# Kernel optimization log

Measured on AMD Instinct MI355X. Metric: run time of the kernel, lower is better.

## Reference

```python
import jax, jax.numpy as jnp
import numpy as np

VOXEL_SIZE = jnp.array([0.075, 0.075], dtype=jnp.float32)
PC_RANGE = jnp.array([-54.0, -54.0], dtype=jnp.float32)
FUSION_STRIDE = 8.0
SRC_STRIDES = (4.0, 8.0)
RADII = (2.4, 4.8)
NSAMPLE = 16
NKEY = 500


def _mlp(x, w1, g1, b1, w2, b2):
    # Linear(no bias) + BatchNorm(eval, running mean=0/var=1 -> affine) + ReLU, then Linear
    h = jax.nn.relu((x @ w1) * g1 + b1)
    return h @ w2 + b2


def _world(coords, stride):
    # voxel coord -> world xy center
    return (coords.astype(jnp.float32) + 0.5) * stride * VOXEL_SIZE + PC_RANGE


def _gather_rows(x, idx):
    # x: (B, N, ...), idx: (B, ...) -> per-batch row gather
    return jax.vmap(lambda f, i: f[i])(x, idx)


def _knn(key_world, src_world, src_feat, radius):
    # key_world (B,Nk,2), src_world (B,Ns,2), src_feat (B,Ns,C)
    d2 = jnp.sum((key_world[:, :, None, :] - src_world[:, None, :, :]) ** 2, axis=-1)  # (B,Nk,Ns)
    d2 = jnp.where(d2 <= radius * radius, d2, jnp.inf)
    negd, idx = jax.lax.top_k(-d2, NSAMPLE)  # nearest NSAMPLE within radius, (B,Nk,K)
    valid = jnp.isfinite(negd).astype(src_feat.dtype)  # empty==0 mask
    feats = _gather_rows(src_feat, idx)  # (B,Nk,K,C)
    return feats * valid[..., None]


def setup_inputs() -> dict:
    key = jax.random.key(0)
    ks = jax.random.split(key, 24)
    s = 0.05
    return {
        'fusion_feat': jax.random.normal(ks[0], (2, 20000, 128), jnp.float32),
        'src_feat_a': jax.random.normal(ks[1], (2, 30000, 128), jnp.float32),
        'src_feat_b': jax.random.normal(ks[2], (2, 30000, 128), jnp.float32),
        'heat_w1': jax.random.normal(ks[3], (128, 128), jnp.float32) * s,
        'heat_g1': jnp.ones((128,), jnp.float32),
        'heat_b1': jnp.zeros((128,), jnp.float32),
        'heat_w2': jax.random.normal(ks[4], (128, 10), jnp.float32) * s,
        'heat_b2': jnp.zeros((10,), jnp.float32),
        'knn_w': jax.random.normal(ks[5], (2, 16), jnp.float32) * s,
        'knn_b': jnp.zeros((2,), jnp.float32),
        'kw_w1': jax.random.normal(ks[6], (128, 64), jnp.float32) * s,
        'kw_g1': jnp.ones((64,), jnp.float32),
        'kw_b1': jnp.zeros((64,), jnp.float32),
        'kw_w2': jax.random.normal(ks[7], (64, 3), jnp.float32) * s,
        'kw_b2': jnp.zeros((3,), jnp.float32),
        'fuse_w1': jax.random.normal(ks[8], (256, 256), jnp.float32) * s,
        'fuse_g1': jnp.ones((256,), jnp.float32),
        'fuse_b1': jnp.zeros((256,), jnp.float32),
        'fuse_w2': jax.random.normal(ks[9], (256, 128), jnp.float32) * s,
        'fuse_b2': jnp.zeros((128,), jnp.float32),
        'fusion_coords': jax.random.randint(ks[10], (2, 20000, 2), 0, 180, jnp.int32),
        'src_coords_a': jax.random.randint(ks[11], (2, 30000, 2), 0, 360, jnp.int32),
        'src_coords_b': jax.random.randint(ks[12], (2, 30000, 2), 0, 180, jnp.int32),
    }


def reference(fusion_feat, src_feat_a, src_feat_b, heat_w1, heat_g1, heat_b1,
              heat_w2, heat_b2, knn_w, knn_b, kw_w1, kw_g1, kw_b1, kw_w2, kw_b2,
              fuse_w1, fuse_g1, fuse_b1, fuse_w2, fuse_b2,
              fusion_coords, src_coords_a, src_coords_b):
    B = fusion_feat.shape[0]
    # heatmap head over all fusion voxels
    scores10 = _mlp(fusion_feat, heat_w1, heat_g1, heat_b1, heat_w2, heat_b2)  # (B,Nf,10)
    heat_scores = jnp.max(scores10, axis=-1)
    cls = jnp.argmax(scores10, axis=-1)
    # per-sample top-k key voxel selection
    _, tki = jax.lax.top_k(jax.nn.sigmoid(heat_scores), NKEY)  # (B,Nk)
    key_feat = _gather_rows(fusion_feat, tki)      # (B,Nk,128)
    key_coords = _gather_rows(fusion_coords, tki)  # (B,Nk,2)
    key_class = _gather_rows(cls, tki)             # (B,Nk)
    key_world = _world(key_coords, FUSION_STRIDE)  # (B,Nk,2)

    srcs = ((src_feat_a, src_coords_a), (src_feat_b, src_coords_b))
    mlp_feats = []
    for s, (sf, sc) in enumerate(srcs):
        sw = _world(sc, SRC_STRIDES[s])
        kf = _knn(key_world, sw, sf, RADII[s])  # (B,Nk,K,C), zeroed where empty
        # Linear over the K neighbor axis (knn_feat_mlp: NSAMPLE -> 1)
        mf = jnp.einsum('bnkc,k->bnc', kf, knn_w[s]) + knn_b[s]
        mlp_feats.append(mf)

    w = jax.nn.softmax(_mlp(key_feat, kw_w1, kw_g1, kw_b1, kw_w2, kw_b2), axis=-1)  # (B,Nk,3)
    # faithful to original: key_voxel_feat is re-scaled cumulatively inside the loop
    kvf = key_feat
    fuse_sum = jnp.zeros_like(key_feat)
    for i in range(len(srcs)):
        kvf = w[..., i:i + 1] * kvf
        fuse_sum = fuse_sum + kvf * mlp_feats[i]
    fused = jnp.concatenate([fuse_sum, kvf], axis=-1)  # (B,Nk,256)
    out = _mlp(fused, fuse_w1, fuse_g1, fuse_b1, fuse_w2, fuse_b2)  # (B,Nk,128)

    bs_col = jnp.broadcast_to(jnp.arange(B, dtype=key_coords.dtype)[:, None, None], (B, NKEY, 1))
    key_voxel_indices = jnp.concatenate([bs_col, key_coords], axis=-1).reshape(B * NKEY, 3)
    return (out.reshape(B * NKEY, -1), key_voxel_indices,
            heat_scores.reshape(-1), scores10.reshape(-1, scores10.shape[-1]), key_class)
```

## Files before the change

### kernel.cpp

```cpp
#include <hip/hip_runtime.h>
#include <math.h>

#define BB 2
#define NF 20000
#define NS 30000
#define CH 128
#define NK 500
#define KNN 16
#define KPB 4

#define HA 2.4024f
#define HB 4.8048f
#define NCA 45
#define NCB 23
#define CELLS_A 2025
#define CELLS_B 529

#define GB 8
#define SLICE 3750
#define SLICE4 1875

#define OUT0_OFF 0
#define OUT1_OFF 128000
#define OUT2_OFF 131000
#define OUT3_OFF 171000
#define OUT4_OFF 571000

#define WS_CLS   0
#define WS_TKI   160000
#define WS_KW    164000
#define WS_MF    172000
#define WS_KEYS  WS_MF
#define WS_BH    492000
#define WS_RAWK  754144
#define WS_GSTART 1196000
#define WS_PTS    1236880
#define WS_PIDX   2196880

#define STB(s,b)  ((s) ? (4052 + (b) * 530) : ((b) * 2026))

__device__ __forceinline__ void fma4(float4& acc, float sc, const float4& wv) {
    acc.x += sc * wv.x; acc.y += sc * wv.y;
    acc.z += sc * wv.z; acc.w += sc * wv.w;
}

__device__ __forceinline__ unsigned ordf(float s) {
    unsigned u = __float_as_uint(s);
    return (u & 0x80000000u) ? ~u : (u | 0x80000000u);
}

__device__ __forceinline__ int cell_of(int cxi, int cyi, float stride, float inv_h,
                                       int nc, float& sx, float& sy)
{
    sx = __fadd_rn(__fmul_rn(__fmul_rn(__fadd_rn((float)cxi, 0.5f), stride), 0.075f), -54.0f);
    sy = __fadd_rn(__fmul_rn(__fmul_rn(__fadd_rn((float)cyi, 0.5f), stride), 0.075f), -54.0f);
    int cx = (int)floorf((sx + 54.0f) * inv_h);
    int cy = (int)floorf((sy + 54.0f) * inv_h);
    cx = min(max(cx, 0), nc - 1);
    cy = min(max(cy, 0), nc - 1);
    return cy * nc + cx;
}

__device__ __forceinline__ unsigned block_scan_incl(unsigned v, int tid,
                                                    volatile unsigned* ws,
                                                    unsigned* total)
{
    const int lane = tid & 63, wid = tid >> 6;
    unsigned p = v;
#pragma unroll
    for (int off = 1; off < 64; off <<= 1) {
        unsigned t = (unsigned)__shfl_up((int)p, off);
        if (lane >= off) p += t;
    }
    __syncthreads();
    if (lane == 63) ws[wid] = p;
    __syncthreads();
    unsigned woff = 0, tot = 0;
#pragma unroll
    for (int w = 0; w < 16; ++w) {
        unsigned s = ws[w];
        tot += s;
        if (w < wid) woff += s;
    }
    *total = tot;
    return p + woff;
}

__global__ __launch_bounds__(256) void heat_kernel(
    const float* __restrict__ x,
    const float* __restrict__ w1,
// ... 115 lines not shown
    }
    __syncthreads();

    const int r = tid >> 2;
    const int p = tid & 3;
    float a2[10];
#pragma unroll
    for (int c = 0; c < 10; ++c) a2[c] = 0.f;
    for (int kk = 0; kk < 32; ++kk) {
        int k = kk * 4 + p;
        float hv = Hs[r * 132 + k];
#pragma unroll
        for (int c = 0; c < 10; ++c) a2[c] += hv * W2s[k * 10 + c];
    }
#pragma unroll
    for (int c = 0; c < 10; ++c) {
        a2[c] += __shfl_xor(a2[c], 1);
        a2[c] += __shfl_xor(a2[c], 2);
    }
    if (p == 0) {
        int m = m0 + r;
        float best = -INFINITY;
        int bi = 0;
#pragma unroll
        for (int c = 0; c < 10; ++c) {
            float s = a2[c] + b2[c];
            out_s10[(size_t)m * 10 + c] = s;
            if (s > best) { best = s; bi = c; }
        }
        out_heat[m] = best;
        cls[m] = bi;
        int b = m / NF;
        unsigned i = (unsigned)(m - b * NF);
        float sig = 1.0f / (1.0f + expf(-best));
        keys[m] = ((unsigned long long)ordf(sig) << 32) | (unsigned)(~i);
        rawk[m] = ordf(best);
    }
}

#define H1BINS 16384

__global__ __launch_bounds__(1024) void mid_kernel(
    const unsigned long long* __restrict__ keys,
    const unsigned* __restrict__ rawk,
    const int* __restrict__ cls,
    const int* __restrict__ fcoords,
    float* __restrict__ out1,
    float* __restrict__ out4,
    int* __restrict__ tki,
    float* __restrict__ keyworld,
    const int* __restrict__ sca, const int* __restrict__ scb,
    const int* __restrict__ bh,
    int* __restrict__ gstart,
    float2* __restrict__ pts, int* __restrict__ pidx)
{
    __shared__ unsigned h[H1BINS];
    __shared__ unsigned long long list[1024];
    __shared__ unsigned short bins16[NF];
    __shared__ unsigned wsum[16];
    __shared__ unsigned chunk_s, aboveC_s, T1_s, aboveT1_s, cand_s, thr_s, cnt_s;
    const int tid = threadIdx.x;
    const int blk = blockIdx.x;

    if (blk >= 2) {
        const int idx = blk - 2;
        const int sb = idx >> 3;
        const int j = idx & (GB - 1);
        const int s = sb >> 1, b = sb & 1;
        const int n = s ? CELLS_B : CELLS_A;
        const int nc = s ? NCB : NCA;
        const float stride = s ? 8.0f : 4.0f;
        const float inv_h = s ? (1.0f / HB) : (1.0f / HA);
        const int stb = STB(s, b);
        const int2* sc = ((const int2*)(s ? scb : sca)) + (size_t)b * NS;
        const int4* scv = (const int4*)sc;
        const size_t pbase = ((size_t)s * BB + b) * NS;
        const int* bhsb = bh + (sb << 14);
        int* tot = (int*)h;
        int* cur = ((int*)h) + 2048;

        for (int c = tid; c < 2048; c += 1024) {
            int t = 0, pr = 0;
#pragma unroll
            for (int g = 0; g < GB; ++g) {
                int v = bhsb[(g << 11) + c];
                t += v;
                if (g < j) pr += v;
            }
            tot[c] = t;
            cur[c] = pr;
        }
        __syncthreads();
        const int i0 = tid * 2, i1 = tid * 2 + 1;
        int c0 = (i0 < n) ? tot[i0] : 0;
        int c1 = (i1 < n) ? tot[i1] : 0;
        unsigned totsum;
        unsigned P = block_scan_incl((unsigned)(c0 + c1), tid, wsum, &totsum);
        const int excl = (int)P - (c0 + c1);
        if (i0 < n) {
            if (j == 0) gstart[stb + i0] = excl;
            cur[i0] += excl;
        }
        if (i1 < n) {
            if (j == 0) gstart[stb + i1] = excl + c0;
            cur[i1] += excl + c0;
        }
        if (j == 0 && tid == 0) gstart[stb + n] = NS;
        __syncthreads();
        for (int p = j * SLICE4 + tid; p < (j + 1) * SLICE4; p += 1024) {
            int4 v = scv[p];
            float sx0, sy0, sx1, sy1;
            int cell0 = cell_of(v.x, v.y, stride, inv_h, nc, sx0, sy0);
            int cell1 = cell_of(v.z, v.w, stride, inv_h, nc, sx1, sy1);
            int pos0 = atomicAdd(&cur[cell0], 1);
            int pos1 = atomicAdd(&cur[cell1], 1);
            pts[pbase + pos0] = make_float2(sx0, sy0);
            pidx[pbase + pos0] = p * 2;
            pts[pbase + pos1] = make_float2(sx1, sy1);
            pidx[pbase + pos1] = p * 2 + 1;
        }
        return;
    }

    const int b = blk;
    const unsigned long long* kb = keys + (size_t)b * NF;
    const unsigned* rk = rawk + (size_t)b * NF;
    const unsigned K = NK;

    for (int i = tid; i < H1BINS; i += 1024) h[i] = 0u;
    __syncthreads();
    for (int i2 = tid; i2 < NF / 2; i2 += 1024) {
        uint2 rv = ((const uint2*)rk)[i2];
        unsigned b0 = rv.x >> 18;
        unsigned b1_ = rv.y >> 18;
        bins16[2 * i2] = (unsigned short)b0;
        bins16[2 * i2 + 1] = (unsigned short)b1_;
        atomicAdd(&h[b0], 1u);
        atomicAdd(&h[b1_], 1u);
    }
    __syncthreads();
    unsigned ck = 0;
    {
        int base = tid * 16;
#pragma unroll
        for (int j = 0; j < 16; ++j) ck += h[base + j];
    }
    {
        unsigned tot;
        unsigned P = block_scan_incl(ck, tid, wsum, &tot);
        unsigned suf = tot - P + ck;
        unsigned above = tot - P;
        if (above < K && K <= suf) { chunk_s = (unsigned)tid; aboveC_s = above; }
    }
    __syncthreads();
    if (tid == 0) {
        int bin = (int)chunk_s * 16 + 15;
        unsigned acc = aboveC_s;
        for (;; --bin) { if (acc + h[bin] >= K) break; acc += h[bin]; }
        T1_s = (unsigned)bin;
        aboveT1_s = acc;
        cand_s = acc + h[bin];
        cnt_s = 0u;
    }
    __syncthreads();
    const unsigned T1 = T1_s;

    if (cand_s <= 1024u) {
        const unsigned* b32v = (const unsigned*)bins16;
        for (int i2 = tid; i2 < NF / 2; i2 += 1024) {
            unsigned pk = b32v[i2];
            if ((pk & 0xFFFFu) >= T1) {
                unsigned pos = atomicAdd(&cnt_s, 1u);
                if (pos < 1024u) list[pos] = kb[2 * i2];
            }
            if ((pk >> 16) >= T1) {
                unsigned pos = atomicAdd(&cnt_s, 1u);
                if (pos < 1024u) list[pos] = kb[2 * i2 + 1];
            }
        }
    } else {
// ... 2 lines not shown
        __syncthreads();
#pragma unroll 4
        for (int i = tid; i < NF; i += 1024) {
            unsigned rw = rk[i];
            if ((rw >> 18) == T1)
                atomicAdd(&h[(rw >> 8) & 1023u], 1u);
        }
        __syncthreads();
        unsigned hb = h[tid];
        {
            unsigned tot2;
            unsigned P2 = block_scan_incl(hb, tid, wsum, &tot2);
            unsigned suf = tot2 - P2 + hb;
            unsigned above = tot2 - P2;
            if (above < K2 && K2 <= suf) thr_s = (T1 << 10) | (unsigned)tid;
        }
        __syncthreads();
        const unsigned thr24 = thr_s;
#pragma unroll 4
        for (int i = tid; i < NF; i += 1024) {
            unsigned rw = rk[i];
            if ((rw >> 8) >= thr24) {
                unsigned pos = atomicAdd(&cnt_s, 1u);
                if (pos < 1024u) list[pos] = kb[i];
            }
        }
    }
    __syncthreads();
    const int cc = (int)(cnt_s > 1024u ? 1024u : cnt_s);

    if (tid < cc) {
        unsigned long long mykey = list[tid];
        unsigned r = 0;
#pragma unroll 8
        for (int j = 0; j < cc; ++j) r += (list[j] > mykey) ? 1u : 0u;
        if (r < (unsigned)NK) {
            int idx = (int)(~(unsigned)(mykey & 0xFFFFFFFFull));
            tki[b * NK + (int)r] = idx;
            int c0 = fcoords[((size_t)b * NF + idx) * 2 + 0];
            int c1 = fcoords[((size_t)b * NF + idx) * 2 + 1];
            size_t o = (size_t)(b * NK + (int)r);
            out1[o * 3 + 0] = (float)b;
            out1[o * 3 + 1] = (float)c0;
            out1[o * 3 + 2] = (float)c1;
            float wx = __fadd_rn(__fmul_rn(__fmul_rn(__fadd_rn((float)c0, 0.5f), 8.0f), 0.075f), -54.0f);
            float wy = __fadd_rn(__fmul_rn(__fmul_rn(__fadd_rn((float)c1, 0.5f), 8.0f), 0.075f), -54.0f);
            keyworld[o * 2 + 0] = wx;
            keyworld[o * 2 + 1] = wy;
            out4[o] = (float)cls[(size_t)b * NF + idx];
        }
    }
}

__global__ __launch_bounds__(256) void knn_kernel(
    const float* __restrict__ sfa, const float* __restrict__ sfb,
    const int* __restrict__ gstart,
    const float2* __restrict__ pts, const int* __restrict__ pidx,
    const float* __restrict__ knn_w,
    const float* __restrict__ knn_b,
    const float* __restrict__ keyworld,
    float* __restrict__ mf)
{
    __shared__ unsigned long long list[1024];
    __shared__ float psum[128];
    __shared__ unsigned cnt_s;
    const int tid = threadIdx.x;
    const int blk = blockIdx.x;
    const int s = blk / (BB * NK);
    const int rest = blk % (BB * NK);
    const int b = rest / NK;
    const int r = rest % NK;
    const float* sfeat = s ? sfb : sfa;
    const float r2 = s ? (float)(4.8 * 4.8) : (float)(2.4 * 2.4);
    const float inv_h = s ? (1.0f / HB) : (1.0f / HA);
    const int nc = s ? NCB : NCA;
    const int stb = STB(s, b);
    const size_t pbase = ((size_t)s * BB + b) * NS;

    if (tid == 0) cnt_s = 0u;
    __syncthreads();
    const float kx = keyworld[((size_t)b * NK + r) * 2 + 0];
    const float ky = keyworld[((size_t)b * NK + r) * 2 + 1];
    int cx = (int)floorf((kx + 54.0f) * inv_h);
    int cy = (int)floorf((ky + 54.0f) * inv_h);
    cx = min(max(cx, 0), nc - 1);
    cy = min(max(cy, 0), nc - 1);
    const int c0 = max(cx - 1, 0), c1 = min(cx + 1, nc - 1);
    const int cy0 = max(cy - 1, 0), cy1 = min(cy + 1, nc - 1);

    for (int cyy = cy0; cyy <= cy1; ++cyy) {
        int lo = gstart[stb + cyy * nc + c0];
        int hi = gstart[stb + cyy * nc + c1 + 1];
        for (int p = lo + tid; p < hi; p += 256) {
            float2 w = pts[pbase + p];
            float dx = __fsub_rn(kx, w.x);
            float dy = __fsub_rn(ky, w.y);
            float d2 = __fadd_rn(__fmul_rn(dx, dx), __fmul_rn(dy, dy));
            if (d2 <= r2) {
                unsigned pos = atomicAdd(&cnt_s, 1u);
                if (pos < 1024u)
                    list[pos] = ((unsigned long long)__float_as_uint(d2) << 32)
                              | (unsigned)pidx[pbase + p];
            }
        }
    }
    __syncthreads();
    int cc = (int)cnt_s;
    if (cc > 1024) cc = 1024;
    int n2 = 16;
    while (n2 < cc) n2 <<= 1;
    for (int i = tid; i < n2; i += 256)
        if (i >= cc) list[i] = ~0ull;
    __syncthreads();
    for (int kk = 2; kk <= n2; kk <<= 1) {
        for (int j = kk >> 1; j > 0; j >>= 1) {
            for (int i = tid; i < n2; i += 256) {
                int ixj = i ^ j;
                if (ixj > i) {
                    unsigned long long a = list[i], bv = list[ixj];
                    bool up = ((i & kk) == 0);
                    bool sw = up ? (a > bv) : (a < bv);
                    if (sw) { list[i] = bv; list[ixj] = a; }
                }
            }
            __syncthreads();
        }
    }
    {
        int K = cc < KNN ? cc : KNN;
        int col = tid & 127, half = tid >> 7;
        float acc = 0.f;
        int k0 = half * 8, k1 = min(K, half * 8 + 8);
        for (int k = k0; k < k1; ++k) {
            unsigned i = (unsigned)(list[k] & 0xFFFFFFFFull);
            acc += knn_w[s * 16 + k] * sfeat[((size_t)b * NS + i) * CH + col];
        }
        if (half) psum[col] = acc;
        __syncthreads();
        if (!half)
            mf[(((size_t)s * BB + b) * NK + r) * CH + col] = knn_b[s] + acc + psum[col];
    }
}

__global__ __launch_bounds__(1024) void fuse_kernel(
    const float* __restrict__ ffeat,
    const int* __restrict__ tki,
    const float* __restrict__ kw_w1, const float* __restrict__ kw_g1,
    const float* __restrict__ kw_b1, const float* __restrict__ kw_w2,
    const float* __restrict__ kw_b2,
    const float* __restrict__ fuse_w1, const float* __restrict__ fuse_g1,
    const float* __restrict__ fuse_b1, const float* __restrict__ fuse_w2,
    const float* __restrict__ fuse_b2,
    const float* __restrict__ mf,
    float* __restrict__ out0)
{
    __shared__ float pL[16384];
    __shared__ float xsT[512];
    __shared__ float mfs[1024];
    __shared__ float fusedvT[1024];
    __shared__ float h2sT[1024];
    __shared__ float prm[964];
    __shared__ float hsX[256];
    __shared__ float p2[96];
    __shared__ float l3[12];
    __shared__ float wsm[8];
    __shared__ int idxs[KPB], bs[KPB], rs[KPB];
    const int tid = threadIdx.x;
    const int f0 = blockIdx.x * KPB;

    if (tid < 964) {
        float v;
        if (tid < 64)       v = kw_g1[tid];
        else if (tid < 128) v = kw_b1[tid - 64];
        else if (tid < 320) v = kw_w2[tid - 128];
        else if (tid < 323) v = kw_b2[tid - 320];
        else if (tid < 324) v = 0.f;
        else if (tid < 580) v = fuse_g1[tid - 324];
        else if (tid < 836) v = fuse_b1[tid - 580];
        else                v = fuse_b2[tid - 836];
        prm[tid] = v;
    }
    if (tid < KPB) {
        int flat = f0 + tid;
        int b = flat / NK;
        bs[tid] = b;
        rs[tid] = flat - b * NK;
        idxs[tid] = tki[flat];
    }
    __syncthreads();

    if (tid < 128) {
        int key = tid >> 5, c4 = tid & 31;
        float4 v = ((const float4*)(ffeat + ((size_t)bs[key] * NF + idxs[key]) * CH))[c4];
        xsT[(c4 * 4 + 0) * 4 + key] = v.x;
        xsT[(c4 * 4 + 1) * 4 + key] = v.y;
        xsT[(c4 * 4 + 2) * 4 + key] = v.z;
        xsT[(c4 * 4 + 3) * 4 + key] = v.w;
    }
    if (tid < 256) {
        int ss = tid >> 7, key = (tid >> 5) & 3, c4 = tid & 31;
        float4 v = ((const float4*)(mf + (((size_t)ss * BB + bs[key]) * NK + rs[key]) * CH))[c4];
        *(float4*)&mfs[ss * 512 + key * 128 + c4 * 4] = v;
    }
    __syncthreads();

    if (tid < 256) {
        const int og = tid & 15, kseg = tid >> 4;
        float4 wr[8];
#pragma unroll
        for (int m = 0; m < 8; ++m)
            wr[m] = ((const float4*)kw_w1)[(kseg * 8 + m) * 16 + og];
        float4 a0 = {0, 0, 0, 0}, a1 = {0, 0, 0, 0}, a2 = {0, 0, 0, 0}, a3 = {0, 0, 0, 0};
#pragma unroll
        for (int m = 0; m < 8; ++m) {
            float4 f4 = *(const float4*)&xsT[(kseg * 8 + m) * 4];
            fma4(a0, f4.x, wr[m]);
            fma4(a1, f4.y, wr[m]);
            fma4(a2, f4.z, wr[m]);
            fma4(a3, f4.w, wr[m]);
        }
        *(float4*)&pL[(kseg * 4 + 0) * 64 + og * 4] = a0;
        *(float4*)&pL[(kseg * 4 + 1) * 64 + og * 4] = a1;
        *(float4*)&pL[(kseg * 4 + 2) * 64 + og * 4] = a2;
        *(float4*)&pL[(kseg * 4 + 3) * 64 + og * 4] = a3;
    }
    __syncthreads();
    if (tid < 256) {
        int out = tid >> 2, key = tid & 3;
        float s = 0.f;
#pragma unroll
        for (int ks = 0; ks < 16; ++ks) s += pL[(ks * 4 + key) * 64 + out];
        float t = s * prm[out] + prm[64 + out];
        hsX[key * 64 + out] = t > 0.f ? t : 0.f;
    }
    __syncthreads();
    if (tid < 96) {
        int key = tid / 24, rr = tid % 24, out = rr >> 3, seg = rr & 7;
        float acc = 0.f;
#pragma unroll
        for (int m = 0; m < 8; ++m) {
            int k = seg * 8 + m;
            acc += hsX[key * 64 + k] * prm[128 + k * 3 + out];
        }
        p2[(key * 3 + out) * 8 + seg] = acc;
    }
    __syncthreads();
    if (tid < 12) {
        int key = tid / 3, out = tid % 3;
        float s = 0.f;
#pragma unroll
        for (int j = 0; j < 8; ++j) s += p2[(key * 3 + out) * 8 + j];
        l3[key * 3 + out] = s + prm[320 + out];
    }
    __syncthreads();
    if (tid < KPB) {
        float l0 = l3[tid * 3], l1 = l3[tid * 3 + 1], l2 = l3[tid * 3 + 2];
        float m = fmaxf(l0, fmaxf(l1, l2));
        float e0 = expf(l0 - m), e1 = expf(l1 - m), e2 = expf(l2 - m);
        float sum = e0 + e1 + e2;
        wsm[tid * 2 + 0] = e0 / sum;
        wsm[tid * 2 + 1] = e1 / sum;
    }
    __syncthreads();

    {
        int c = tid >> 2, key = tid & 3;
        float w0 = wsm[key * 2], w1_ = wsm[key * 2 + 1];
        float val;
        if (c < 128) {
            float xv_ = xsT[c * 4 + key];
            float m0 = mfs[key * 128 + c];
            float m1 = mfs[512 + key * 128 + c];
            float kv = w0 * xv_;
            float kv2 = w1_ * kv;
            val = kv * m0 + kv2 * m1;
        } else {
            float xv_ = xsT[(c - 128) * 4 + key];
            val = w1_ * (w0 * xv_);
        }
        fusedvT[tid] = val;
    }
    __syncthreads();

    {
        const int og = tid & 63, kseg = tid >> 6;
        const float4* w1v = (const float4*)fuse_w1;
        float4 wr[16];
#pragma unroll
        for (int m = 0; m < 16; ++m)
            wr[m] = w1v[(kseg * 16 + m) * 64 + og];
        float4 a0 = {0, 0, 0, 0}, a1 = {0, 0, 0, 0}, a2 = {0, 0, 0, 0}, a3 = {0, 0, 0, 0};
#pragma unroll
        for (int m = 0; m < 16; ++m) {
            float4 f4 = *(const float4*)&fusedvT[(kseg * 16 + m) * 4];
            fma4(a0, f4.x, wr[m]);
            fma4(a1, f4.y, wr[m]);
            fma4(a2, f4.z, wr[m]);
            fma4(a3, f4.w, wr[m]);
        }
        *(float4*)&pL[(kseg * 4 + 0) * 256 + og * 4] = a0;
        *(float4*)&pL[(kseg * 4 + 1) * 256 + og * 4] = a1;
        *(float4*)&pL[(kseg * 4 + 2) * 256 + og * 4] = a2;
        *(float4*)&pL[(kseg * 4 + 3) * 256 + og * 4] = a3;
    }
    __syncthreads();
    {
        int out = tid >> 2, key = tid & 3;
        float s = 0.f;
#pragma unroll
        for (int ks = 0; ks < 16; ++ks) s += pL[(ks * 4 + key) * 256 + out];
        float t = s * prm[324 + out] + prm[580 + out];
        h2sT[out * 4 + key] = t > 0.f ? t : 0.f;
    }
    __syncthreads();

    {
        const int og2 = tid & 31, kseg2 = tid >> 5;
        const float4* w2v = (const float4*)fuse_w2;
        float4 wr[8];
#pragma unroll
        for (int m = 0; m < 8; ++m)
            wr[m] = w2v[(kseg2 * 8 + m) * 32 + og2];
        float4 a0 = {0, 0, 0, 0}, a1 = {0, 0, 0, 0}, a2 = {0, 0, 0, 0}, a3 = {0, 0, 0, 0};
#pragma unroll
        for (int m = 0; m < 8; ++m) {
            float4 f4 = *(const float4*)&h2sT[(kseg2 * 8 + m) * 4];
            fma4(a0, f4.x, wr[m]);
            fma4(a1, f4.y, wr[m]);
            fma4(a2, f4.z, wr[m]);
            fma4(a3, f4.w, wr[m]);
        }
        *(float4*)&pL[(kseg2 * 4 + 0) * 128 + og2 * 4] = a0;
        *(float4*)&pL[(kseg2 * 4 + 1) * 128 + og2 * 4] = a1;
        *(float4*)&pL[(kseg2 * 4 + 2) * 128 + og2 * 4] = a2;
        *(float4*)&pL[(kseg2 * 4 + 3) * 128 + og2 * 4] = a3;
    }
    __syncthreads();
    if (tid < 512) {
        int out = tid >> 2, key = tid & 3;
        float s = prm[836 + out];
#pragma unroll
        for (int ks = 0; ks < 32; ++ks) s += pL[(ks * 4 + key) * 128 + out];
        out0[((size_t)bs[key] * NK + rs[key]) * CH + out] = s;
    }
}

extern "C" void kernel_launch(void* const* d_in, const int* in_sizes, int n_in,
                              void* d_out, int out_size, void* d_ws, size_t ws_size,
                              hipStream_t stream)
{
    const float* fusion_feat = (const float*)d_in[0];
    const float* src_feat_a  = (const float*)d_in[1];
    const float* src_feat_b  = (const float*)d_in[2];
    const float* heat_w1 = (const float*)d_in[3];
    const float* heat_g1 = (const float*)d_in[4];
    const float* heat_b1 = (const float*)d_in[5];
    const float* heat_w2 = (const float*)d_in[6];
    const float* heat_b2 = (const float*)d_in[7];
    const float* knn_w   = (const float*)d_in[8];
    const float* knn_b   = (const float*)d_in[9];
    const float* kw_w1   = (const float*)d_in[10];
    const float* kw_g1   = (const float*)d_in[11];
    const float* kw_b1   = (const float*)d_in[12];
    const float* kw_w2   = (const float*)d_in[13];
    const float* kw_b2   = (const float*)d_in[14];
    const float* fuse_w1 = (const float*)d_in[15];
    const float* fuse_g1 = (const float*)d_in[16];
    const float* fuse_b1 = (const float*)d_in[17];
    const float* fuse_w2 = (const float*)d_in[18];
    const float* fuse_b2 = (const float*)d_in[19];
    const int* fusion_coords = (const int*)d_in[20];
    const int* src_coords_a  = (const int*)d_in[21];
    const int* src_coords_b  = (const int*)d_in[22];

    float* out = (float*)d_out;
    char* ws = (char*)d_ws;
    int* cls = (int*)(ws + WS_CLS);
    int* tki = (int*)(ws + WS_TKI);
    float* keyworld = (float*)(ws + WS_KW);
    float* mf = (float*)(ws + WS_MF);
    unsigned long long* keys = (unsigned long long*)(ws + WS_KEYS);
    int* bh = (int*)(ws + WS_BH);
    unsigned* rawk = (unsigned*)(ws + WS_RAWK);
    int* gstart = (int*)(ws + WS_GSTART);
    float2* pts = (float2*)(ws + WS_PTS);
    int* pidx = (int*)(ws + WS_PIDX);

    heat_kernel<<<(BB * NF) / 64 + 4 * GB, 256, 0, stream>>>(
        fusion_feat, heat_w1, heat_g1, heat_b1, heat_w2, heat_b2,
        out + OUT2_OFF, out + OUT3_OFF, cls, keys,
        src_coords_a, src_coords_b, bh, rawk);

    mid_kernel<<<2 + 4 * GB, 1024, 0, stream>>>(
        keys, rawk, cls, fusion_coords,
        out + OUT1_OFF, out + OUT4_OFF, tki, keyworld,
        src_coords_a, src_coords_b, bh, gstart, pts, pidx);

    knn_kernel<<<2 * BB * NK, 256, 0, stream>>>(
        src_feat_a, src_feat_b, gstart, pts, pidx,
        knn_w, knn_b, keyworld, mf);

    fuse_kernel<<<(BB * NK) / KPB, 1024, 0, stream>>>(
        fusion_feat, tki, kw_w1, kw_g1, kw_b1, kw_w2, kw_b2,
        fuse_w1, fuse_g1, fuse_b1, fuse_w2, fuse_b2, mf, out + OUT0_OFF);
}
```

Measured before the change: 218.5 us.

## Fuse fuse MLP into knn kernel via per-key completion counter

Removes the separate fuse_kernel launch. Each knn block atomically increments a per-key counter, which mid_kernel resets. The second block to finish for a key (covering both source scales) runs the key-weight MLP, softmax, fusion and two-layer MLP for that single key using 256 threads. This saves a kernel launch and the tail gap between launches. In exchange, weights are no longer shared across four keys per block, so fuse_w1 and fuse_w2 are reloaded per key, and a serial tail of matrix work now runs inside the last-finishing knn blocks.

Result: slower. 438.6 us (+100.7%).

```diff
diff --git a/kernel.cpp b/kernel.cpp
--- a/kernel.cpp
+++ b/kernel.cpp
@@ -7,7 +7,6 @@
 #define CH 128
 #define NK 500
 #define KNN 16
-#define KPB 4
 
 #define HA 2.4024f
 #define HB 4.8048f
@@ -36,6 +35,7 @@
 #define WS_GSTART 1196000
 #define WS_PTS    1236880
 #define WS_PIDX   2196880
+#define WS_KDONE  2676880
 
 #define STB(s,b)  ((s) ? (4052 + (b) * 530) : ((b) * 2026))
 
@@ -257,7 +257,8 @@
     const int* __restrict__ sca, const int* __restrict__ scb,
     const int* __restrict__ bh,
     int* __restrict__ gstart,
-    float2* __restrict__ pts, int* __restrict__ pidx)
+    float2* __restrict__ pts, int* __restrict__ pidx,
+    unsigned* __restrict__ kdone)
 {
     __shared__ unsigned h[H1BINS];
     __shared__ unsigned long long list[1024];
@@ -331,6 +332,8 @@
     const unsigned long long* kb = keys + (size_t)b * NF;
     const unsigned* rk = rawk + (size_t)b * NF;
     const unsigned K = NK;
+
+    if (tid < NK) kdone[b * NK + tid] = 0u;
 
     for (int i = tid; i < H1BINS; i += 1024) h[i] = 0u;
     __syncthreads();
@@ -446,11 +449,34 @@
     const float* __restrict__ knn_w,
     const float* __restrict__ knn_b,
     const float* __restrict__ keyworld,
-    float* __restrict__ mf)
+    float* __restrict__ mf,
+    const float* __restrict__ ffeat,
+    const int* __restrict__ tki,
+    const float* __restrict__ kw_w1, const float* __restrict__ kw_g1,
+    const float* __restrict__ kw_b1, const float* __restrict__ kw_w2,
+    const float* __restrict__ kw_b2,
+    const float* __restrict__ fuse_w1, const float* __restrict__ fuse_g1,
+    const float* __restrict__ fuse_b1, const float* __restrict__ fuse_w2,
+    const float* __restrict__ fuse_b2,
+    unsigned* __restrict__ kdone,
+    float* __restrict__ out0)
 {
-    __shared__ unsigned long long list[1024];
+    __shared__ union {
+        unsigned long long list[1024];
+        struct {
+            float prm[964];
+            float xs[128];
+            float mfs[256];
+            float fusedv[256];
+            float hs[64];
+            float h2[256];
+        } f;
+    } u;
+    __shared__ float pbuf[1024];
     __shared__ float psum[128];
+    __shared__ float p2[24], l3[3], wsm[2];
     __shared__ unsigned cnt_s;
+    __shared__ int old_s;
     const int tid = threadIdx.x;
     const int blk = blockIdx.x;
     const int s = blk / (BB * NK);
@@ -486,8 +512,8 @@
             if (d2 <= r2) {
                 unsigned pos = atomicAdd(&cnt_s, 1u);
                 if (pos < 1024u)
-                    list[pos] = ((unsigned long long)__float_as_uint(d2) << 32)
-                              | (unsigned)pidx[pbase + p];
+                    u.list[pos] = ((unsigned long long)__float_as_uint(d2) << 32)
+                                | (unsigned)pidx[pbase + p];
             }
         }
     }
@@ -497,17 +523,17 @@
     int n2 = 16;
     while (n2 < cc) n2 <<= 1;
     for (int i = tid; i < n2; i += 256)
-        if (i >= cc) list[i] = ~0ull;
+        if (i >= cc) u.list[i] = ~0ull;
     __syncthreads();
     for (int kk = 2; kk <= n2; kk <<= 1) {
         for (int j = kk >> 1; j > 0; j >>= 1) {
             for (int i = tid; i < n2; i += 256) {
                 int ixj = i ^ j;
                 if (ixj > i) {
-                    unsigned long long a = list[i], bv = list[ixj];
+                    unsigned long long a = u.list[i], bv = u.list[ixj];
                     bool up = ((i & kk) == 0);
                     bool sw = up ? (a > bv) : (a < bv);
-                    if (sw) { list[i] = bv; list[ixj] = a; }
+                    if (sw) { u.list[i] = bv; u.list[ixj] = a; }
                 }
             }
             __syncthreads();
@@ -519,7 +545,7 @@
         float acc = 0.f;
         int k0 = half * 8, k1 = min(K, half * 8 + 8);
         for (int k = k0; k < k1; ++k) {
-            unsigned i = (unsigned)(list[k] & 0xFFFFFFFFull);
+            unsigned i = (unsigned)(u.list[k] & 0xFFFFFFFFull);
             acc += knn_w[s * 16 + k] * sfeat[((size_t)b * NS + i) * CH + col];
         }
         if (half) psum[col] = acc;
@@ -527,208 +553,133 @@
         if (!half)
             mf[(((size_t)s * BB + b) * NK + r) * CH + col] = knn_b[s] + acc + psum[col];
     }
-}
-
-__global__ __launch_bounds__(1024) void fuse_kernel(
-    const float* __restrict__ ffeat,
-    const int* __restrict__ tki,
-    const float* __restrict__ kw_w1, const float* __restrict__ kw_g1,
-    const float* __restrict__ kw_b1, const float* __restrict__ kw_w2,
-    const float* __restrict__ kw_b2,
-    const float* __restrict__ fuse_w1, const float* __restrict__ fuse_g1,
-    const float* __restrict__ fuse_b1, const float* __restrict__ fuse_w2,
-    const float* __restrict__ fuse_b2,
-    const float* __restrict__ mf,
-    float* __restrict__ out0)
-{
-    __shared__ float pL[16384];
-    __shared__ float xsT[512];
-    __shared__ float mfs[1024];
-    __shared__ float fusedvT[1024];
-    __shared__ float h2sT[1024];
-    __shared__ float prm[964];
-    __shared__ float hsX[256];
-    __shared__ float p2[96];
-    __shared__ float l3[12];
-    __shared__ float wsm[8];
-    __shared__ int idxs[KPB], bs[KPB], rs[KPB];
-    const int tid = threadIdx.x;
-    const int f0 = blockIdx.x * KPB;
-
-    if (tid < 964) {
+
+    __syncthreads();
+    __threadfence();
+    if (tid == 0) old_s = (int)atomicAdd(&kdone[b * NK + r], 1u);
+    __syncthreads();
+    if (old_s != 1) return;
+    __threadfence();
+
+    for (int i = tid; i < 964; i += 256) {
         float v;
-        if (tid < 64)       v = kw_g1[tid];
-        else if (tid < 128) v = kw_b1[tid - 64];
-        else if (tid < 320) v = kw_w2[tid - 128];
-        else if (tid < 323) v = kw_b2[tid - 320];
-        else if (tid < 324) v = 0.f;
-        else if (tid < 580) v = fuse_g1[tid - 324];
-        else if (tid < 836) v = fuse_b1[tid - 580];
-        else                v = fuse_b2[tid - 836];
-        prm[tid] = v;
-    }
-    if (tid < KPB) {
-        int flat = f0 + tid;
-        int b = flat / NK;
-        bs[tid] = b;
-        rs[tid] = flat - b * NK;
-        idxs[tid] = tki[flat];
-    }
-    __syncthreads();
-
-    if (tid < 128) {
-        int key = tid >> 5, c4 = tid & 31;
-        float4 v = ((const float4*)(ffeat + ((size_t)bs[key] * NF + idxs[key]) * CH))[c4];
-        xsT[(c4 * 4 + 0) * 4 + key] = v.x;
-        xsT[(c4 * 4 + 1) * 4 + key] = v.y;
-        xsT[(c4 * 4 + 2) * 4 + key] = v.z;
-        xsT[(c4 * 4 + 3) * 4 + key] = v.w;
-    }
-    if (tid < 256) {
-        int ss = tid >> 7, key = (tid >> 5) & 3, c4 = tid & 31;
-        float4 v = ((const float4*)(mf + (((size_t)ss * BB + bs[key]) * NK + rs[key]) * CH))[c4];
-        *(float4*)&mfs[ss * 512 + key * 128 + c4 * 4] = v;
-    }
-    __syncthreads();
-
-    if (tid < 256) {
+        if (i < 64)       v = kw_g1[i];
+        else if (i < 128) v = kw_b1[i - 64];
+        else if (i < 320) v = kw_w2[i - 128];
+        else if (i < 323) v = kw_b2[i - 320];
+        else if (i < 324) v = 0.f;
+        else if (i < 580) v = fuse_g1[i - 324];
+        else if (i < 836) v = fuse_b1[i - 580];
+        else              v = fuse_b2[i - 836];
+        u.f.prm[i] = v;
+    }
+    const int kidx = tki[b * NK + r];
+    if (tid < 32) {
+        float4 v = ((const float4*)(ffeat + ((size_t)b * NF + kidx) * CH))[tid];
+        *(float4*)&u.f.xs[tid * 4] = v;
+    }
+    if (tid < 64) {
+        int ss = tid >> 5, c4 = tid & 31;
+        float4 v = ((const float4*)(mf + (((size_t)ss * BB + b) * NK + r) * CH))[c4];
+        *(float4*)&u.f.mfs[ss * 128 + c4 * 4] = v;
+    }
+    __syncthreads();
+
+    {
         const int og = tid & 15, kseg = tid >> 4;
-        float4 wr[8];
-#pragma unroll
-        for (int m = 0; m < 8; ++m)
-            wr[m] = ((const float4*)kw_w1)[(kseg * 8 + m) * 16 + og];
-        float4 a0 = {0, 0, 0, 0}, a1 = {0, 0, 0, 0}, a2 = {0, 0, 0, 0}, a3 = {0, 0, 0, 0};
+        float4 a = {0, 0, 0, 0};
 #pragma unroll
         for (int m = 0; m < 8; ++m) {
-            float4 f4 = *(const float4*)&xsT[(kseg * 8 + m) * 4];
-            fma4(a0, f4.x, wr[m]);
-            fma4(a1, f4.y, wr[m]);
-            fma4(a2, f4.z, wr[m]);
-            fma4(a3, f4.w, wr[m]);
-        }
-        *(float4*)&pL[(kseg * 4 + 0) * 64 + og * 4] = a0;
-        *(float4*)&pL[(kseg * 4 + 1) * 64 + og * 4] = a1;
-        *(float4*)&pL[(kseg * 4 + 2) * 64 + og * 4] = a2;
-        *(float4*)&pL[(kseg * 4 + 3) * 64 + og * 4] = a3;
-    }
-    __syncthreads();
-    if (tid < 256) {
-        int out = tid >> 2, key = tid & 3;
-        float s = 0.f;
-#pragma unroll
-        for (int ks = 0; ks < 16; ++ks) s += pL[(ks * 4 + key) * 64 + out];
-        float t = s * prm[out] + prm[64 + out];
-        hsX[key * 64 + out] = t > 0.f ? t : 0.f;
-    }
-    __syncthreads();
-    if (tid < 96) {
-        int key = tid / 24, rr = tid % 24, out = rr >> 3, seg = rr & 7;
+            float4 wr = ((const float4*)kw_w1)[(kseg * 8 + m) * 16 + og];
+            fma4(a, u.f.xs[kseg * 8 + m], wr);
+        }
+        *(float4*)&pbuf[kseg * 64 + og * 4] = a;
+    }
+    __syncthreads();
+    if (tid < 64) {
+        float sum = 0.f;
+#pragma unroll
+        for (int ks = 0; ks < 16; ++ks) sum += pbuf[ks * 64 + tid];
+        float t = sum * u.f.prm[tid] + u.f.prm[64 + tid];
+        u.f.hs[tid] = t > 0.f ? t : 0.f;
+    }
+    __syncthreads();
+    if (tid < 24) {
+        int out = tid >> 3, seg = tid & 7;
         float acc = 0.f;
 #pragma unroll
         for (int m = 0; m < 8; ++m) {
             int k = seg * 8 + m;
-            acc += hsX[key * 64 + k] * prm[128 + k * 3 + out];
-        }
-        p2[(key * 3 + out) * 8 + seg] = acc;
-    }
-    __syncthreads();
-    if (tid < 12) {
-        int key = tid / 3, out = tid % 3;
-        float s = 0.f;
-#pragma unroll
-        for (int j = 0; j < 8; ++j) s += p2[(key * 3 + out) * 8 + j];
-        l3[key * 3 + out] = s + prm[320 + out];
-    }
-    __syncthreads();
-    if (tid < KPB) {
-        float l0 = l3[tid * 3], l1 = l3[tid * 3 + 1], l2 = l3[tid * 3 + 2];
-        float m = fmaxf(l0, fmaxf(l1, l2));
-        float e0 = expf(l0 - m), e1 = expf(l1 - m), e2 = expf(l2 - m);
+            acc += u.f.hs[k] * u.f.prm[128 + k * 3 + out];
+        }
+        p2[out * 8 + seg] = acc;
+    }
+    __syncthreads();
+    if (tid < 3) {
+        float sum = 0.f;
+#pragma unroll
+        for (int j = 0; j < 8; ++j) sum += p2[tid * 8 + j];
+        l3[tid] = sum + u.f.prm[320 + tid];
+    }
+    __syncthreads();
+    if (tid == 0) {
+        float l0 = l3[0], l1 = l3[1], l2 = l3[2];
+        float mx = fmaxf(l0, fmaxf(l1, l2));
+        float e0 = expf(l0 - mx), e1 = expf(l1 - mx), e2 = expf(l2 - mx);
         float sum = e0 + e1 + e2;
-        wsm[tid * 2 + 0] = e0 / sum;
-        wsm[tid * 2 + 1] = e1 / sum;
-    }
-    __syncthreads();
-
+        wsm[0] = e0 / sum;
+        wsm[1] = e1 / sum;
+    }
+    __syncthreads();
     {
-        int c = tid >> 2, key = tid & 3;
-        float w0 = wsm[key * 2], w1_ = wsm[key * 2 + 1];
+        int c = tid;
+        float w0 = wsm[0], w1_ = wsm[1];
         float val;
         if (c < 128) {
-            float xv_ = xsT[c * 4 + key];
-            float m0 = mfs[key * 128 + c];
-            float m1 = mfs[512 + key * 128 + c];
-            float kv = w0 * xv_;
+            float xv = u.f.xs[c];
+            float kv = w0 * xv;
             float kv2 = w1_ * kv;
-            val = kv * m0 + kv2 * m1;
+            val = kv * u.f.mfs[c] + kv2 * u.f.mfs[128 + c];
         } else {
-            float xv_ = xsT[(c - 128) * 4 + key];
-            val = w1_ * (w0 * xv_);
-        }
-        fusedvT[tid] = val;
-    }
-    __syncthreads();
-
+            val = w1_ * (w0 * u.f.xs[c - 128]);
+        }
+        u.f.fusedv[c] = val;
+    }
+    __syncthreads();
     {
         const int og = tid & 63, kseg = tid >> 6;
-        const float4* w1v = (const float4*)fuse_w1;
-        float4 wr[16];
-#pragma unroll
-        for (int m = 0; m < 16; ++m)
-            wr[m] = w1v[(kseg * 16 + m) * 64 + og];
-        float4 a0 = {0, 0, 0, 0}, a1 = {0, 0, 0, 0}, a2 = {0, 0, 0, 0}, a3 = {0, 0, 0, 0};
-#pragma unroll
-        for (int m = 0; m < 16; ++m) {
-            float4 f4 = *(const float4*)&fusedvT[(kseg * 16 + m) * 4];
-            fma4(a0, f4.x, wr[m]);
-            fma4(a1, f4.y, wr[m]);
-            fma4(a2, f4.z, wr[m]);
-            fma4(a3, f4.w, wr[m]);
-        }
-        *(float4*)&pL[(kseg * 4 + 0) * 256 + og * 4] = a0;
-        *(float4*)&pL[(kseg * 4 + 1) * 256 + og * 4] = a1;
-        *(float4*)&pL[(kseg * 4 + 2) * 256 + og * 4] = a2;
-        *(float4*)&pL[(kseg * 4 + 3) * 256 + og * 4] = a3;
+        float4 a = {0, 0, 0, 0};
+        for (int m = 0; m < 64; ++m) {
+            float4 wr = ((const float4*)fuse_w1)[(kseg * 64 + m) * 64 + og];
+            fma4(a, u.f.fusedv[kseg * 64 + m], wr);
+        }
+        *(float4*)&pbuf[kseg * 256 + og * 4] = a;
     }
     __syncthreads();
     {
-        int out = tid >> 2, key = tid & 3;
-        float s = 0.f;
-#pragma unroll
-        for (int ks = 0; ks < 16; ++ks) s += pL[(ks * 4 + key) * 256 + out];
-        float t = s * prm[324 + out] + prm[580 + out];
-        h2sT[out * 4 + key] = t > 0.f ? t : 0.f;
-    }
-    __syncthreads();
-
+        int out = tid;
+        float sum = 0.f;
+#pragma unroll
+        for (int ks = 0; ks < 4; ++ks) sum += pbuf[ks * 256 + out];
+        float t = sum * u.f.prm[324 + out] + u.f.prm[580 + out];
+        u.f.h2[out] = t > 0.f ? t : 0.f;
+    }
+    __syncthreads();
     {
         const int og2 = tid & 31, kseg2 = tid >> 5;
-        const float4* w2v = (const float4*)fuse_w2;
-        float4 wr[8];
-#pragma unroll
-        for (int m = 0; m < 8; ++m)
-            wr[m] = w2v[(kseg2 * 8 + m) * 32 + og2];
-        float4 a0 = {0, 0, 0, 0}, a1 = {0, 0, 0, 0}, a2 = {0, 0, 0, 0}, a3 = {0, 0, 0, 0};
-#pragma unroll
-        for (int m = 0; m < 8; ++m) {
-            float4 f4 = *(const float4*)&h2sT[(kseg2 * 8 + m) * 4];
-            fma4(a0, f4.x, wr[m]);
-            fma4(a1, f4.y, wr[m]);
-            fma4(a2, f4.z, wr[m]);
-            fma4(a3, f4.w, wr[m]);
-        }
-        *(float4*)&pL[(kseg2 * 4 + 0) * 128 + og2 * 4] = a0;
-        *(float4*)&pL[(kseg2 * 4 + 1) * 128 + og2 * 4] = a1;
-        *(float4*)&pL[(kseg2 * 4 + 2) * 128 + og2 * 4] = a2;
-        *(float4*)&pL[(kseg2 * 4 + 3) * 128 + og2 * 4] = a3;
-    }
-    __syncthreads();
-    if (tid < 512) {
-        int out = tid >> 2, key = tid & 3;
-        float s = prm[836 + out];
-#pragma unroll
-        for (int ks = 0; ks < 32; ++ks) s += pL[(ks * 4 + key) * 128 + out];
-        out0[((size_t)bs[key] * NK + rs[key]) * CH + out] = s;
+        float4 a = {0, 0, 0, 0};
+        for (int m = 0; m < 32; ++m) {
+            float4 wr = ((const float4*)fuse_w2)[(kseg2 * 32 + m) * 32 + og2];
+            fma4(a, u.f.h2[kseg2 * 32 + m], wr);
+        }
+        *(float4*)&pbuf[kseg2 * 128 + og2 * 4] = a;
+    }
+    __syncthreads();
+    if (tid < 128) {
+        float sum = u.f.prm[836 + tid];
+#pragma unroll
+        for (int ks = 0; ks < 8; ++ks) sum += pbuf[ks * 128 + tid];
+        out0[((size_t)b * NK + r) * CH + tid] = sum;
     }
 }
 
@@ -772,6 +723,7 @@
     int* gstart = (int*)(ws + WS_GSTART);
     float2* pts = (float2*)(ws + WS_PTS);
     int* pidx = (int*)(ws + WS_PIDX);
+    unsigned* kdone = (unsigned*)(ws + WS_KDONE);
 
     heat_kernel<<<(BB * NF) / 64 + 4 * GB, 256, 0, stream>>>(
         fusion_feat, heat_w1, heat_g1, heat_b1, heat_w2, heat_b2,
@@ -781,13 +733,12 @@
     mid_kernel<<<2 + 4 * GB, 1024, 0, stream>>>(
         keys, rawk, cls, fusion_coords,
         out + OUT1_OFF, out + OUT4_OFF, tki, keyworld,
-        src_coords_a, src_coords_b, bh, gstart, pts, pidx);
+        src_coords_a, src_coords_b, bh, gstart, pts, pidx, kdone);
 
     knn_kernel<<<2 * BB * NK, 256, 0, stream>>>(
         src_feat_a, src_feat_b, gstart, pts, pidx,
-        knn_w, knn_b, keyworld, mf);
-
-    fuse_kernel<<<(BB * NK) / KPB, 1024, 0, stream>>>(
+        knn_w, knn_b, keyworld, mf,
         fusion_feat, tki, kw_w1, kw_g1, kw_b1, kw_w2, kw_b2,
-        fuse_w1, fuse_g1, fuse_b1, fuse_w2, fuse_b2, mf, out + OUT0_OFF);
+        fuse_w1, fuse_g1, fuse_b1, fuse_w2, fuse_b2,
+        kdone, out + OUT0_OFF);
 }
```

## Fuse KNN neighbor search into fuse kernel with per-key 128-thread groups

Applied to the files above, without the earlier changes.

Merges the KNN kernel into the fuse kernel: each 1024-thread block handles 4 keys × 2 sources, with 128-thread groups doing the grid search, bitonic sort and weighted gather directly into shared memory. This removes one kernel launch and the global round-trip of the mlp feature buffer. In exchange, the grid shrinks from 2000 blocks of 256 threads to 250 blocks, the per-list neighbor cap drops from 1024 to 512, and all groups sort to the largest count in the block. That may reduce parallelism and latency hiding in the search phase.

Result: no change. 220.4 us (+0.9%).

```diff
diff --git a/kernel.cpp b/kernel.cpp
--- a/kernel.cpp
+++ b/kernel.cpp
@@ -29,8 +29,8 @@
 #define WS_CLS   0
 #define WS_TKI   160000
 #define WS_KW    164000
-#define WS_MF    172000
-#define WS_KEYS  WS_MF
+#define WS_SCRATCH 172000
+#define WS_KEYS  WS_SCRATCH
 #define WS_BH    492000
 #define WS_RAWK  754144
 #define WS_GSTART 1196000
@@ -439,97 +439,13 @@
     }
 }
 
-__global__ __launch_bounds__(256) void knn_kernel(
+__global__ __launch_bounds__(1024) void knnfuse_kernel(
     const float* __restrict__ sfa, const float* __restrict__ sfb,
     const int* __restrict__ gstart,
     const float2* __restrict__ pts, const int* __restrict__ pidx,
     const float* __restrict__ knn_w,
     const float* __restrict__ knn_b,
     const float* __restrict__ keyworld,
-    float* __restrict__ mf)
-{
-    __shared__ unsigned long long list[1024];
-    __shared__ float psum[128];
-    __shared__ unsigned cnt_s;
-    const int tid = threadIdx.x;
-    const int blk = blockIdx.x;
-    const int s = blk / (BB * NK);
-    const int rest = blk % (BB * NK);
-    const int b = rest / NK;
-    const int r = rest % NK;
-    const float* sfeat = s ? sfb : sfa;
-    const float r2 = s ? (float)(4.8 * 4.8) : (float)(2.4 * 2.4);
-    const float inv_h = s ? (1.0f / HB) : (1.0f / HA);
-    const int nc = s ? NCB : NCA;
-    const int stb = STB(s, b);
-    const size_t pbase = ((size_t)s * BB + b) * NS;
-
-    if (tid == 0) cnt_s = 0u;
-    __syncthreads();
-    const float kx = keyworld[((size_t)b * NK + r) * 2 + 0];
-    const float ky = keyworld[((size_t)b * NK + r) * 2 + 1];
-    int cx = (int)floorf((kx + 54.0f) * inv_h);
-    int cy = (int)floorf((ky + 54.0f) * inv_h);
-    cx = min(max(cx, 0), nc - 1);
-    cy = min(max(cy, 0), nc - 1);
-    const int c0 = max(cx - 1, 0), c1 = min(cx + 1, nc - 1);
-    const int cy0 = max(cy - 1, 0), cy1 = min(cy + 1, nc - 1);
-
-    for (int cyy = cy0; cyy <= cy1; ++cyy) {
-        int lo = gstart[stb + cyy * nc + c0];
-        int hi = gstart[stb + cyy * nc + c1 + 1];
-        for (int p = lo + tid; p < hi; p += 256) {
-            float2 w = pts[pbase + p];
-            float dx = __fsub_rn(kx, w.x);
-            float dy = __fsub_rn(ky, w.y);
-            float d2 = __fadd_rn(__fmul_rn(dx, dx), __fmul_rn(dy, dy));
-            if (d2 <= r2) {
-                unsigned pos = atomicAdd(&cnt_s, 1u);
-                if (pos < 1024u)
-                    list[pos] = ((unsigned long long)__float_as_uint(d2) << 32)
-                              | (unsigned)pidx[pbase + p];
-            }
-        }
-    }
-    __syncthreads();
-    int cc = (int)cnt_s;
-    if (cc > 1024) cc = 1024;
-    int n2 = 16;
-    while (n2 < cc) n2 <<= 1;
-    for (int i = tid; i < n2; i += 256)
-        if (i >= cc) list[i] = ~0ull;
-    __syncthreads();
-    for (int kk = 2; kk <= n2; kk <<= 1) {
-        for (int j = kk >> 1; j > 0; j >>= 1) {
-            for (int i = tid; i < n2; i += 256) {
-                int ixj = i ^ j;
-                if (ixj > i) {
-                    unsigned long long a = list[i], bv = list[ixj];
-                    bool up = ((i & kk) == 0);
-                    bool sw = up ? (a > bv) : (a < bv);
-                    if (sw) { list[i] = bv; list[ixj] = a; }
-                }
-            }
-            __syncthreads();
-        }
-    }
-    {
-        int K = cc < KNN ? cc : KNN;
-        int col = tid & 127, half = tid >> 7;
-        float acc = 0.f;
-        int k0 = half * 8, k1 = min(K, half * 8 + 8);
-        for (int k = k0; k < k1; ++k) {
-            unsigned i = (unsigned)(list[k] & 0xFFFFFFFFull);
-            acc += knn_w[s * 16 + k] * sfeat[((size_t)b * NS + i) * CH + col];
-        }
-        if (half) psum[col] = acc;
-        __syncthreads();
-        if (!half)
-            mf[(((size_t)s * BB + b) * NK + r) * CH + col] = knn_b[s] + acc + psum[col];
-    }
-}
-
-__global__ __launch_bounds__(1024) void fuse_kernel(
     const float* __restrict__ ffeat,
     const int* __restrict__ tki,
     const float* __restrict__ kw_w1, const float* __restrict__ kw_g1,
@@ -538,10 +454,12 @@
     const float* __restrict__ fuse_w1, const float* __restrict__ fuse_g1,
     const float* __restrict__ fuse_b1, const float* __restrict__ fuse_w2,
     const float* __restrict__ fuse_b2,
-    const float* __restrict__ mf,
     float* __restrict__ out0)
 {
-    __shared__ float pL[16384];
+    __shared__ union {
+        float pL[16384];
+        unsigned long long list[4096];
+    } u;
     __shared__ float xsT[512];
     __shared__ float mfs[1024];
     __shared__ float fusedvT[1024];
@@ -552,8 +470,14 @@
     __shared__ float l3[12];
     __shared__ float wsm[8];
     __shared__ int idxs[KPB], bs[KPB], rs[KPB];
+    __shared__ unsigned jcnt[8];
     const int tid = threadIdx.x;
     const int f0 = blockIdx.x * KPB;
+
+    const int jid = tid >> 7;
+    const int jtid = tid & 127;
+    const int jkey = jid >> 1;
+    const int js = jid & 1;
 
     if (tid < 964) {
         float v;
@@ -574,6 +498,7 @@
         rs[tid] = flat - b * NK;
         idxs[tid] = tki[flat];
     }
+    if (tid < 8) jcnt[tid] = 0u;
     __syncthreads();
 
     if (tid < 128) {
@@ -584,10 +509,87 @@
         xsT[(c4 * 4 + 2) * 4 + key] = v.z;
         xsT[(c4 * 4 + 3) * 4 + key] = v.w;
     }
-    if (tid < 256) {
-        int ss = tid >> 7, key = (tid >> 5) & 3, c4 = tid & 31;
-        float4 v = ((const float4*)(mf + (((size_t)ss * BB + bs[key]) * NK + rs[key]) * CH))[c4];
-        *(float4*)&mfs[ss * 512 + key * 128 + c4 * 4] = v;
+
+    {
+        const int b = bs[jkey], r = rs[jkey];
+        const float r2 = js ? (float)(4.8 * 4.8) : (float)(2.4 * 2.4);
+        const float inv_h = js ? (1.0f / HB) : (1.0f / HA);
+        const int nc = js ? NCB : NCA;
+        const int stb = STB(js, b);
+        const size_t pbase = ((size_t)js * BB + b) * NS;
+        unsigned long long* jlist = u.list + (jid << 9);
+
+        const float kx = keyworld[((size_t)b * NK + r) * 2 + 0];
+        const float ky = keyworld[((size_t)b * NK + r) * 2 + 1];
+        int cx = (int)floorf((kx + 54.0f) * inv_h);
+        int cy = (int)floorf((ky + 54.0f) * inv_h);
+        cx = min(max(cx, 0), nc - 1);
+        cy = min(max(cy, 0), nc - 1);
+        const int c0 = max(cx - 1, 0), c1 = min(cx + 1, nc - 1);
+        const int cy0 = max(cy - 1, 0), cy1 = min(cy + 1, nc - 1);
+
+        for (int cyy = cy0; cyy <= cy1; ++cyy) {
+            int lo = gstart[stb + cyy * nc + c0];
+            int hi = gstart[stb + cyy * nc + c1 + 1];
+            for (int p = lo + jtid; p < hi; p += 128) {
+                float2 w = pts[pbase + p];
+                float dx = __fsub_rn(kx, w.x);
+                float dy = __fsub_rn(ky, w.y);
+                float d2 = __fadd_rn(__fmul_rn(dx, dx), __fmul_rn(dy, dy));
+                if (d2 <= r2) {
+                    unsigned pos = atomicAdd(&jcnt[jid], 1u);
+                    if (pos < 512u)
+                        jlist[pos] = ((unsigned long long)__float_as_uint(d2) << 32)
+                                   | (unsigned)pidx[pbase + p];
+                }
+            }
+        }
+    }
+    __syncthreads();
+
+    int maxcc = 0;
+#pragma unroll
+    for (int g = 0; g < 8; ++g) {
+        int c = (int)jcnt[g];
+        if (c > 512) c = 512;
+        maxcc = max(maxcc, c);
+    }
+    int n2 = 16;
+    while (n2 < maxcc) n2 <<= 1;
+    const int myc = min((int)jcnt[jid], 512);
+    {
+        unsigned long long* jlist = u.list + (jid << 9);
+        for (int i = jtid; i < n2; i += 128)
+            if (i >= myc) jlist[i] = ~0ull;
+    }
+    __syncthreads();
+    for (int kk = 2; kk <= n2; kk <<= 1) {
+        for (int j = kk >> 1; j > 0; j >>= 1) {
+            unsigned long long* jlist = u.list + (jid << 9);
+            for (int i = jtid; i < n2; i += 128) {
+                int ixj = i ^ j;
+                if (ixj > i) {
+                    unsigned long long a = jlist[i], bv = jlist[ixj];
+                    bool up = ((i & kk) == 0);
+                    bool sw = up ? (a > bv) : (a < bv);
+                    if (sw) { jlist[i] = bv; jlist[ixj] = a; }
+                }
+            }
+            __syncthreads();
+        }
+    }
+
+    {
+        const int b = bs[jkey];
+        const float* sfeat = js ? sfb : sfa;
+        unsigned long long* jlist = u.list + (jid << 9);
+        int K = myc < KNN ? myc : KNN;
+        float acc = 0.f;
+        for (int k = 0; k < K; ++k) {
+            unsigned i = (unsigned)(jlist[k] & 0xFFFFFFFFull);
+            acc += knn_w[js * 16 + k] * sfeat[((size_t)b * NS + i) * CH + jtid];
+        }
+        mfs[js * 512 + jkey * 128 + jtid] = knn_b[js] + acc;
     }
     __syncthreads();
 
@@ -606,17 +608,17 @@
             fma4(a2, f4.z, wr[m]);
             fma4(a3, f4.w, wr[m]);
         }
-        *(float4*)&pL[(kseg * 4 + 0) * 64 + og * 4] = a0;
-        *(float4*)&pL[(kseg * 4 + 1) * 64 + og * 4] = a1;
-        *(float4*)&pL[(kseg * 4 + 2) * 64 + og * 4] = a2;
-        *(float4*)&pL[(kseg * 4 + 3) * 64 + og * 4] = a3;
+        *(float4*)&u.pL[(kseg * 4 + 0) * 64 + og * 4] = a0;
+        *(float4*)&u.pL[(kseg * 4 + 1) * 64 + og * 4] = a1;
+        *(float4*)&u.pL[(kseg * 4 + 2) * 64 + og * 4] = a2;
+        *(float4*)&u.pL[(kseg * 4 + 3) * 64 + og * 4] = a3;
     }
     __syncthreads();
     if (tid < 256) {
         int out = tid >> 2, key = tid & 3;
         float s = 0.f;
 #pragma unroll
-        for (int ks = 0; ks < 16; ++ks) s += pL[(ks * 4 + key) * 64 + out];
+        for (int ks = 0; ks < 16; ++ks) s += u.pL[(ks * 4 + key) * 64 + out];
         float t = s * prm[out] + prm[64 + out];
         hsX[key * 64 + out] = t > 0.f ? t : 0.f;
     }
@@ -685,17 +687,17 @@
             fma4(a2, f4.z, wr[m]);
             fma4(a3, f4.w, wr[m]);
         }
-        *(float4*)&pL[(kseg * 4 + 0) * 256 + og * 4] = a0;
-        *(float4*)&pL[(kseg * 4 + 1) * 256 + og * 4] = a1;
-        *(float4*)&pL[(kseg * 4 + 2) * 256 + og * 4] = a2;
-        *(float4*)&pL[(kseg * 4 + 3) * 256 + og * 4] = a3;
+        *(float4*)&u.pL[(kseg * 4 + 0) * 256 + og * 4] = a0;
+        *(float4*)&u.pL[(kseg * 4 + 1) * 256 + og * 4] = a1;
+        *(float4*)&u.pL[(kseg * 4 + 2) * 256 + og * 4] = a2;
+        *(float4*)&u.pL[(kseg * 4 + 3) * 256 + og * 4] = a3;
     }
     __syncthreads();
     {
         int out = tid >> 2, key = tid & 3;
         float s = 0.f;
 #pragma unroll
-        for (int ks = 0; ks < 16; ++ks) s += pL[(ks * 4 + key) * 256 + out];
+        for (int ks = 0; ks < 16; ++ks) s += u.pL[(ks * 4 + key) * 256 + out];
         float t = s * prm[324 + out] + prm[580 + out];
         h2sT[out * 4 + key] = t > 0.f ? t : 0.f;
     }
@@ -717,17 +719,17 @@
             fma4(a2, f4.z, wr[m]);
             fma4(a3, f4.w, wr[m]);
         }
-        *(float4*)&pL[(kseg2 * 4 + 0) * 128 + og2 * 4] = a0;
-        *(float4*)&pL[(kseg2 * 4 + 1) * 128 + og2 * 4] = a1;
-        *(float4*)&pL[(kseg2 * 4 + 2) * 128 + og2 * 4] = a2;
-        *(float4*)&pL[(kseg2 * 4 + 3) * 128 + og2 * 4] = a3;
+        *(float4*)&u.pL[(kseg2 * 4 + 0) * 128 + og2 * 4] = a0;
+        *(float4*)&u.pL[(kseg2 * 4 + 1) * 128 + og2 * 4] = a1;
+        *(float4*)&u.pL[(kseg2 * 4 + 2) * 128 + og2 * 4] = a2;
+        *(float4*)&u.pL[(kseg2 * 4 + 3) * 128 + og2 * 4] = a3;
     }
     __syncthreads();
     if (tid < 512) {
         int out = tid >> 2, key = tid & 3;
         float s = prm[836 + out];
 #pragma unroll
-        for (int ks = 0; ks < 32; ++ks) s += pL[(ks * 4 + key) * 128 + out];
+        for (int ks = 0; ks < 32; ++ks) s += u.pL[(ks * 4 + key) * 128 + out];
         out0[((size_t)bs[key] * NK + rs[key]) * CH + out] = s;
     }
 }
@@ -765,7 +767,6 @@
     int* cls = (int*)(ws + WS_CLS);
     int* tki = (int*)(ws + WS_TKI);
     float* keyworld = (float*)(ws + WS_KW);
-    float* mf = (float*)(ws + WS_MF);
     unsigned long long* keys = (unsigned long long*)(ws + WS_KEYS);
     int* bh = (int*)(ws + WS_BH);
     unsigned* rawk = (unsigned*)(ws + WS_RAWK);
@@ -783,11 +784,10 @@
         out + OUT1_OFF, out + OUT4_OFF, tki, keyworld,
         src_coords_a, src_coords_b, bh, gstart, pts, pidx);
 
-    knn_kernel<<<2 * BB * NK, 256, 0, stream>>>(
+    knnfuse_kernel<<<(BB * NK) / KPB, 1024, 0, stream>>>(
         src_feat_a, src_feat_b, gstart, pts, pidx,
-        knn_w, knn_b, keyworld, mf);
-
-    fuse_kernel<<<(BB * NK) / KPB, 1024, 0, stream>>>(
+        knn_w, knn_b, keyworld,
         fusion_feat, tki, kw_w1, kw_g1, kw_b1, kw_w2, kw_b2,
-        fuse_w1, fuse_g1, fuse_b1, fuse_w2, fuse_b2, mf, out + OUT0_OFF);
+        fuse_w1, fuse_g1, fuse_b1, fuse_w2, fuse_b2,
+        out + OUT0_OFF);
 }
```
